# Kernel optimization log

Measured on AMD Instinct MI355X. Metric: run time of the kernel, lower is better.

## Reference

```python
import jax, jax.numpy as jnp
import numpy as np
from jax import lax

B, H, W, C = 16, 56, 56, 256
NH = 8
KD = C // NH  # key/head dim = 32
FF = 1024
EPS = 1e-6
SCALE = KD ** -0.5


def _layernorm(x, g, b):
    m = jnp.mean(x, axis=-1, keepdims=True)
    v = jnp.mean(jnp.square(x - m), axis=-1, keepdims=True)
    return (x - m) * lax.rsqrt(v + EPS) * g + b


def _dwconv(x, w, b):
    # x: (B,H,W,Cd), w: (kh,kw,1,Cd) depthwise (groups = Cd), stride 1, SAME padding
    return lax.conv_general_dilated(
        x, w, window_strides=(1, 1), padding='SAME',
        dimension_numbers=('NHWC', 'HWIO', 'NHWC'),
        feature_group_count=x.shape[-1]) + b


def setup_inputs() -> dict:
    key = jax.random.key(0)
    ks = jax.random.split(key, 20)
    r = lambda i, shape, s=0.02: jax.random.normal(ks[i], shape, jnp.float32) * s
    return {
        'x': jax.random.normal(ks[0], (B, H, W, C), jnp.float32),
        'mask_h': jax.random.normal(ks[1], (NH, H, H), jnp.float32),
        'mask_w': jax.random.normal(ks[2], (NH, W, W), jnp.float32),
        # pos: DWConv2d(C, 3, 1, 1)
        'pos_w': r(3, (3, 3, 1, C)), 'pos_b': jnp.zeros((C,), jnp.float32),
        # retention layer norm
        'ln1_g': jnp.ones((C,), jnp.float32), 'ln1_b': jnp.zeros((C,), jnp.float32),
        # MaSA projections (stored as (in, out) so y = x @ W + b)
        'q_w': r(4, (C, C)), 'q_b': jnp.zeros((C,), jnp.float32),
        'k_w': r(5, (C, C)), 'k_b': jnp.zeros((C,), jnp.float32),
        'v_w': r(6, (C, C)), 'v_b': jnp.zeros((C,), jnp.float32),
        # lepe: DWConv2d(C, 5, 1, 2)
        'lepe_w': r(7, (5, 5, 1, C)), 'lepe_b': jnp.zeros((C,), jnp.float32),
        'out_w': r(8, (C, C)), 'out_b': jnp.zeros((C,), jnp.float32),
        # final layer norm
        'ln2_g': jnp.ones((C,), jnp.float32), 'ln2_b': jnp.zeros((C,), jnp.float32),
        # FFN
        'fc1_w': r(9, (C, FF)), 'fc1_b': jnp.zeros((FF,), jnp.float32),
        'fc2_w': r(10, (FF, C)), 'fc2_b': jnp.zeros((C,), jnp.float32),
    }


def _masa(x, mask_h, mask_w, q_w, q_b, k_w, k_b, v_w, v_b, lepe_w, lepe_b, out_w, out_b):
    b, h, w, _ = x.shape
    q = x @ q_w + q_b
    k = (x @ k_w + k_b) * SCALE
    v = x @ v_w + v_b
    lepe = _dwconv(v, lepe_w, lepe_b)
    qh = q.reshape(b, h, w, NH, KD)
    kh = k.reshape(b, h, w, NH, KD)
    vh = v.reshape(b, h, w, NH, KD)
    # width-axis retention: scores (b, h, NH, w, w), mask_w broadcasts as (NH, w, w)
    attn_w = jax.nn.softmax(jnp.einsum('bhqnd,bhknd->bhnqk', qh, kh) + mask_w, axis=-1)
    vw = jnp.einsum('bhnqk,bhknd->bhnqd', attn_w, vh)  # (b, h, NH, w, KD)
    # height-axis retention: scores (b, w, NH, h, h), mask_h broadcasts as (NH, h, h)
    attn_h = jax.nn.softmax(jnp.einsum('bqwnd,bkwnd->bwnqk', qh, kh) + mask_h, axis=-1)
    out = jnp.einsum('bwnqk,bknwd->bqwnd', attn_h, vw)  # (b, h, w, NH, KD)
    out = out.reshape(b, h, w, NH * KD) + lepe
    return out @ out_w + out_b


def reference(x, mask_h, mask_w, pos_w, pos_b, ln1_g, ln1_b,
              q_w, q_b, k_w, k_b, v_w, v_b, lepe_w, lepe_b, out_w, out_b,
              ln2_g, ln2_b, fc1_w, fc1_b, fc2_w, fc2_b):
    # RetBlock (retention='whole', no layerscale, no dropout / drop_path)
    x = x + _dwconv(x, pos_w, pos_b)
    x = x + _masa(_layernorm(x, ln1_g, ln1_b), mask_h, mask_w,
                  q_w, q_b, k_w, k_b, v_w, v_b, lepe_w, lepe_b, out_w, out_b)
    y = _layernorm(x, ln2_g, ln2_b)
    y = jax.nn.gelu(y @ fc1_w + fc1_b, approximate=False) @ fc2_w + fc2_b
    return x + y
```

## Files before the change

kernel.cpp:

```cpp
#include <hip/hip_runtime.h>
#include <hip/hip_bf16.h>
#include <math.h>
#include <stdint.h>

typedef __bf16 bf16;
typedef __bf16 bf16x8 __attribute__((ext_vector_type(8)));
typedef __bf16 bf16x4 __attribute__((ext_vector_type(4)));
typedef float f32x4 __attribute__((ext_vector_type(4)));

#define AS1 __attribute__((address_space(1)))
#define AS3 __attribute__((address_space(3)))

#define NPIX (16*56*56)
#define CH 256
#define SCALE_K 0.17677669529663687f

__device__ __forceinline__ float gelu_fast(float vv) {
    float t = vv * (-2.30220781f + -0.10294330f * vv * vv);
    float e = __builtin_amdgcn_exp2f(t);
    return vv * __builtin_amdgcn_rcpf(1.0f + e);
}

__global__ __launch_bounds__(256) void prep_kernel(
    const float* __restrict__ q_w, const float* __restrict__ k_w,
    const float* __restrict__ v_w, const float* __restrict__ out_w,
    const float* __restrict__ fc1_w, const float* __restrict__ fc2_w,
    const float* __restrict__ qb, const float* __restrict__ kb,
    const float* __restrict__ vb,
    bf16* __restrict__ wt_qkv, bf16* __restrict__ wt_out,
    bf16* __restrict__ wt_fc1, bf16* __restrict__ wt_fc2,
    float* __restrict__ qkvb)
{
    int idx = blockIdx.x * 256 + threadIdx.x;
    if (idx < 262144) {
        int w = idx >> 16;
        int j = idx & 65535;
        int n = j >> 8, k = j & 255;
        const float* src = (w == 0) ? q_w : (w == 1) ? k_w : (w == 2) ? v_w : out_w;
        float scale = (w == 1) ? SCALE_K : 1.0f;
        bf16* dst = (w < 3) ? (wt_qkv + w * 65536) : wt_out;
        dst[j] = (bf16)(src[k * 256 + n] * scale);
    } else if (idx < 524288) {
        int j = idx - 262144;
        int n = j >> 8, k = j & 255;
        wt_fc1[j] = (bf16)(fc1_w[k * 1024 + n]);
    } else if (idx < 786432) {
        int j = idx - 524288;
        int n = j >> 10, k = j & 1023;
        wt_fc2[j] = (bf16)(fc2_w[k * 256 + n]);
    } else if (idx < 787200) {
        int i = idx - 786432;
        qkvb[i] = (i < 256) ? qb[i] : (i < 512) ? kb[i - 256] * SCALE_K : vb[i - 512];
    }
}

__global__ __launch_bounds__(256) void posconv_ln_kernel(
    const float* __restrict__ x, const float* __restrict__ w,
    const float* __restrict__ bias, const float* __restrict__ g,
    const float* __restrict__ bta, float* __restrict__ x1,
    bf16* __restrict__ tln)
{
    const int wave = threadIdx.x >> 6, lane = threadIdx.x & 63;
    const long pix = (long)blockIdx.x * 4 + wave;
    const int ww = (int)(pix % 56);
    const int hh = (int)((pix / 56) % 56);
    const int b  = (int)(pix / 3136);
    const int c  = lane * 4;
    float4 acc = ((const float4*)(bias + c))[0];
    float4 xin = ((const float4*)(x + pix * 256 + c))[0];
    acc.x += xin.x; acc.y += xin.y; acc.z += xin.z; acc.w += xin.w;
    #pragma unroll
    for (int dh = 0; dh < 3; ++dh) {
        int h2 = hh + dh - 1;
        if (h2 < 0 || h2 >= 56) continue;
        #pragma unroll
        for (int dw = 0; dw < 3; ++dw) {
            int w2 = ww + dw - 1;
            if (w2 < 0 || w2 >= 56) continue;
            float4 xv = ((const float4*)(x + (((long)(b * 56 + h2)) * 56 + w2) * 256 + c))[0];
            float4 wv = ((const float4*)(w + (dh * 3 + dw) * 256 + c))[0];
            acc.x += xv.x * wv.x; acc.y += xv.y * wv.y;
            acc.z += xv.z * wv.z; acc.w += xv.w * wv.w;
        }
    }
    ((float4*)(x1 + pix * 256 + c))[0] = acc;
    float s  = acc.x + acc.y + acc.z + acc.w;
    float q2 = acc.x * acc.x + acc.y * acc.y + acc.z * acc.z + acc.w * acc.w;
    #pragma unroll
    for (int o = 32; o; o >>= 1) {
        s  += __shfl_xor(s,  o, 64);
        q2 += __shfl_xor(q2, o, 64);
    }
    float mean = s * (1.0f / 256.0f);
    float var  = q2 * (1.0f / 256.0f) - mean * mean;
    float rs   = rsqrtf(var + 1e-6f);
    float4 gv = ((const float4*)g)[lane];
    float4 bv = ((const float4*)bta)[lane];
    bf16* o4 = tln + pix * 256 + c;
    o4[0] = (bf16)((acc.x - mean) * rs * gv.x + bv.x);
    o4[1] = (bf16)((acc.y - mean) * rs * gv.y + bv.y);
    o4[2] = (bf16)((acc.z - mean) * rs * gv.z + bv.z);
    o4[3] = (bf16)((acc.w - mean) * rs * gv.w + bv.w);
}

__global__ __launch_bounds__(256) void lepe_kernel(
    const bf16* __restrict__ vpl, const float* __restrict__ w,
    const float* __restrict__ bias, bf16* __restrict__ out)
{
    long idx = (long)blockIdx.x * 256 + threadIdx.x;
    int c8 = (int)(idx & 31);
    long pix = idx >> 5;
    int ww = (int)(pix % 56);
    int hh = (int)((pix / 56) % 56);
    int b  = (int)(pix / 3136);
    int c  = c8 * 8;
    float acc[8];
    #pragma unroll
    for (int j = 0; j < 8; ++j) acc[j] = bias[c + j];
    #pragma unroll
    for (int dh = 0; dh < 5; ++dh) {
        int h2 = hh + dh - 2;
        if (h2 < 0 || h2 >= 56) continue;
        #pragma unroll
        for (int dw = 0; dw < 5; ++dw) {
            int w2 = ww + dw - 2;
            if (w2 < 0 || w2 >= 56) continue;
            bf16x8 vv = *(const bf16x8*)(vpl + (((long)(b * 56 + h2)) * 56 + w2) * 256 + c);
            const float4* wp = (const float4*)(w + (dh * 5 + dw) * 256 + c);
            float4 w0 = wp[0], w1 = wp[1];
            acc[0] += (float)vv[0] * w0.x; acc[1] += (float)vv[1] * w0.y;
            acc[2] += (float)vv[2] * w0.z; acc[3] += (float)vv[3] * w0.w;
            acc[4] += (float)vv[4] * w1.x; acc[5] += (float)vv[5] * w1.y;
            acc[6] += (float)vv[6] * w1.z; acc[7] += (float)vv[7] * w1.w;
        }
    }
    bf16* o = out + pix * 256 + c;
    #pragma unroll
    for (int j = 0; j < 8; ++j) o[j] = (bf16)acc[j];
}

template<bool WIDTH>
__global__ __launch_bounds__(256) void attn_mfma_kernel(
    const bf16* __restrict__ qp, const bf16* __restrict__ kp,
    const bf16* __restrict__ vsrc, const float* __restrict__ mask,
    const bf16* __restrict__ lepe, bf16* __restrict__ outp)
{
    __shared__ bf16 VtAll[4][32][72];
    __shared__ bf16 PlAll[4][16][72];
    const int tid = threadIdx.x;
    const int wave = tid >> 6, lane = tid & 63;
    const int g = lane >> 4, ql = lane & 15;
    const int n  = blockIdx.x / 224;
    const int s  = (blockIdx.x % 224) * 4 + wave;
    const int b  = s / 56, rc = s % 56;
    bf16 (*Vt)[72] = VtAll[wave];
    bf16 (*Pl)[72] = PlAll[wave];
    const long basePix = WIDTH ? ((long)(b * 56 + rc)) * 56 : (long)b * 3136 + rc;
    const long pixStride = WIDTH ? 1 : 56;
    const long stride = pixStride * 256;
    const bf16* qb = qp + basePix * 256 + n * 32;
    const bf16* kb = kp + basePix * 256 + n * 32;
    const bf16* vbp = vsrc + basePix * 256 + n * 32;

    #pragma unroll
    for (int it = 0; it < 2; ++it) {
        int idx = it * 64 + lane;
        if (idx < 112) {
            int pp = idx >> 2, chunk = idx & 3;
            int pos0 = pp * 2;
            bf16x8 v0 = *(const bf16x8*)(vbp + (long)pos0 * stride + chunk * 8);
            bf16x8 v1 = *(const bf16x8*)(vbp + (long)(pos0 + 1) * stride + chunk * 8);
            int colb = pos0 ^ (chunk << 3);
            #pragma unroll
            for (int j = 0; j < 8; ++j) {
                union { bf16 h[2]; unsigned int u; } pk;
                pk.h[0] = v0[j]; pk.h[1] = v1[j];
                *(unsigned int*)&Vt[chunk * 8 + j][colb] = pk.u;
            }
        }
    }
    if (lane < 32) {
        int d = lane;
        int colb = 56 ^ ((d >> 3) << 3);
        *(float4*)&Vt[d][colb] = (float4){0.f, 0.f, 0.f, 0.f};
    }

    bf16x8 qf[4], kf[4];
    #pragma unroll
    for (int t4 = 0; t4 < 4; ++t4) {
        int row = ql + 16 * t4; if (row > 55) row = 55;
        qf[t4] = *(const bf16x8*)(qb + (long)row * stride + 8 * g);
        kf[t4] = *(const bf16x8*)(kb + (long)row * stride + 8 * g);
    }

    f32x4 sA[4][4];
    #pragma unroll
    for (int qt = 0; qt < 4; ++qt)
        #pragma unroll
        for (int kt = 0; kt < 4; ++kt)
            sA[qt][kt] = __builtin_amdgcn_mfma_f32_16x16x32_bf16(
                kf[kt], qf[qt], (f32x4){0.f, 0.f, 0.f, 0.f}, 0, 0, 0);

    const float* mrow = mask + n * 3136;
    #pragma unroll
    for (int qt = 0; qt < 4; ++qt) {
        int qm = ql + 16 * qt; if (qm > 55) qm = 55;
        #pragma unroll
        for (int kt = 0; kt < 4; ++kt) {
            if (kt == 3 && g >= 2) {
                sA[qt][3][0] = -3.0e38f; sA[qt][3][1] = -3.0e38f;
                sA[qt][3][2] = -3.0e38f; sA[qt][3][3] = -3.0e38f;
            } else {
                float4 mv = *(const float4*)(mrow + qm * 56 + kt * 16 + 4 * g);
                sA[qt][kt][0] += mv.x; sA[qt][kt][1] += mv.y;
                sA[qt][kt][2] += mv.z; sA[qt][kt][3] += mv.w;
            }
        }
    }

    #pragma unroll
    for (int qt = 0; qt < 4; ++qt) {
        float m = -3.0e38f;
        #pragma unroll
        for (int kt = 0; kt < 4; ++kt)
            #pragma unroll
            for (int r = 0; r < 4; ++r) m = fmaxf(m, sA[qt][kt][r]);
        m = fmaxf(m, __shfl_xor(m, 16, 64));
        m = fmaxf(m, __shfl_xor(m, 32, 64));
        float p[4][4];
        float sum = 0.f;
        #pragma unroll
        for (int kt = 0; kt < 4; ++kt)
            #pragma unroll
            for (int r = 0; r < 4; ++r) {
                float e = exp2f((sA[qt][kt][r] - m) * 1.4426950408889634f);
                p[kt][r] = e; sum += e;
            }
        sum += __shfl_xor(sum, 16, 64);
        sum += __shfl_xor(sum, 32, 64);
        float rinv = 1.0f / sum;
        #pragma unroll
        for (int kt = 0; kt < 4; ++kt) {
            bf16x4 w;
            #pragma unroll
            for (int r = 0; r < 4; ++r) w[r] = (bf16)(p[kt][r] * rinv);
            *(bf16x4*)&Pl[ql][kt * 16 + 4 * g] = w;
        }
        #pragma unroll
        for (int nt = 0; nt < 2; ++nt) {
            f32x4 o = {0.f, 0.f, 0.f, 0.f};
            #pragma unroll
            for (int ks = 0; ks < 2; ++ks) {
                bf16x8 af = *(const bf16x8*)&Pl[ql][ks * 32 + 8 * g];
                int vrow = ql + 16 * nt;
                int vcol = (ks * 32 + 8 * g) ^ ((vrow >> 3) << 3);
                bf16x8 bv = *(const bf16x8*)&Vt[vrow][vcol];
                o = __builtin_amdgcn_mfma_f32_16x16x32_bf16(af, bv, o, 0, 0, 0);
            }
            if (!(qt == 3 && g >= 2)) {
                #pragma unroll
                for (int r = 0; r < 4; ++r) {
                    int q = 16 * qt + 4 * g + r;
                    long addr = (basePix + (long)q * pixStride) * 256 + n * 32 + nt * 16 + ql;
                    float vv = o[r];
                    if (!WIDTH) vv += (float)lepe[addr];
                    outp[addr] = (bf16)vv;
                }
            }
        }
    }
}

template<bool GELU, bool RESID, bool OUT_BF16, bool QKV3>
__global__ __launch_bounds__(512) void gemm_kernel(
    const bf16* __restrict__ A, const bf16* __restrict__ Wt,
    const float* __restrict__ bias, const float* __restrict__ resid,
    void* __restrict__ Cout, int M, int N, int K)
{
    __shared__ bf16 As[256 * 64];
    __shared__ bf16 Bs[128 * 64];
    const int t = threadIdx.x;
    const int wave = t >> 6, lane = t & 63;
    const int nTilesN = N >> 7;
    const int q8 = gridDim.x >> 3;
    const int o = ((int)blockIdx.x & 7) * q8 + ((int)blockIdx.x >> 3);
    const int tm = o / nTilesN, tn = o % nTilesN;
    const long m0 = (long)tm * 256, n0 = (long)tn * 128;
    const int waveM = (wave >> 1) * 64, waveN = (wave & 1) * 64;
    f32x4 acc[4][4] = {};

    for (int k0 = 0; k0 < K; k0 += 64) {
        #pragma unroll
        for (int i = 0; i < 4; ++i) {
            int c = i * 512 + t;
            int r = c >> 3, cc = (c & 7) * 8;
            const bf16* ga = A + (m0 + r) * (long)K + k0 + cc;
            __builtin_amdgcn_global_load_lds(
                (const AS1 void*)ga, (AS3 void*)(As + c * 8), 16, 0, 0);
        }
        #pragma unroll
        for (int i = 0; i < 2; ++i) {
            int c = i * 512 + t;
            int r = c >> 3, cc = (c & 7) * 8;
            const bf16* gb = Wt + (n0 + r) * (long)K + k0 + cc;
            __builtin_amdgcn_global_load_lds(
                (const AS1 void*)gb, (AS3 void*)(Bs + c * 8), 16, 0, 0);
        }
        __syncthreads();
        #pragma unroll
        for (int kk = 0; kk < 2; ++kk) {
            bf16x8 af[4], bfr[4];
            const int krow = kk * 32 + (lane >> 4) * 8;
            #pragma unroll
            for (int fm = 0; fm < 4; ++fm)
                af[fm] = *(const bf16x8*)&As[(waveM + fm * 16 + (lane & 15)) * 64 + krow];
            #pragma unroll
            for (int fn = 0; fn < 4; ++fn)
                bfr[fn] = *(const bf16x8*)&Bs[(waveN + fn * 16 + (lane & 15)) * 64 + krow];
            #pragma unroll
            for (int fm = 0; fm < 4; ++fm)
                #pragma unroll
                for (int fn = 0; fn < 4; ++fn)
                    acc[fm][fn] = __builtin_amdgcn_mfma_f32_16x16x32_bf16(
                        af[fm], bfr[fn], acc[fm][fn], 0, 0, 0);
        }
        __syncthreads();
    }

    #pragma unroll
    for (int fm = 0; fm < 4; ++fm) {
        #pragma unroll
        for (int r = 0; r < 4; ++r) {
            const long m = m0 + waveM + fm * 16 + (lane >> 4) * 4 + r;
            #pragma unroll
            for (int fn = 0; fn < 4; ++fn) {
                const long n = n0 + waveN + fn * 16 + (lane & 15);
                float vv = acc[fm][fn][r] + bias[n];
                if (GELU)  vv = gelu_fast(vv);
                if (RESID) vv += resid[m * N + n];
                if (QKV3) {
                    long pl = n >> 8;
                    ((bf16*)Cout)[pl * (long)NPIX * 256 + m * 256 + (n & 255)] = (bf16)vv;
                } else if (OUT_BF16) {
                    ((bf16*)Cout)[m * N + n] = (bf16)vv;
                } else {
                    ((float*)Cout)[m * N + n] = vv;
                }
            }
        }
    }
}

__global__ __launch_bounds__(256) void outln_kernel(
    const bf16* __restrict__ A, const bf16* __restrict__ Wt,
    const float* __restrict__ bias, const float* __restrict__ resid,
    const float* __restrict__ g2, const float* __restrict__ b2,
    float* __restrict__ x2out, bf16* __restrict__ uout)
{
    __shared__ bf16 As[64 * 64];
    __shared__ bf16 Bs[256 * 64];
    const int t = threadIdx.x;
    const int wave = t >> 6, lane = t & 63;
    const int g = lane >> 4, ql = lane & 15;
    const int q8 = gridDim.x >> 3;
    const int o = ((int)blockIdx.x & 7) * q8 + ((int)blockIdx.x >> 3);
    const long m0 = (long)o * 64;
    const int waveM = wave * 16;
    f32x4 acc[16] = {};

    for (int k0 = 0; k0 < 256; k0 += 64) {
        #pragma unroll
        for (int i = 0; i < 2; ++i) {
            int c = i * 256 + wave * 64 + lane;
            int r = c >> 3, cc = (c & 7) * 8;
            const bf16* ga = A + (m0 + r) * 256 + k0 + cc;
            __builtin_amdgcn_global_load_lds(
                (const AS1 void*)ga,
                (AS3 void*)(As + (i * 256 + wave * 64) * 8), 16, 0, 0);
        }
        #pragma unroll
        for (int i = 0; i < 8; ++i) {
            int c = i * 256 + wave * 64 + lane;
            int r = c >> 3, cc = (c & 7) * 8;
            const bf16* gb = Wt + r * 256 + k0 + cc;
            __builtin_amdgcn_global_load_lds(
                (const AS1 void*)gb,
                (AS3 void*)(Bs + (i * 256 + wave * 64) * 8), 16, 0, 0);
        }
        __syncthreads();
        #pragma unroll
        for (int kk = 0; kk < 2; ++kk) {
            const int krow = kk * 32 + g * 8;
            bf16x8 af = *(const bf16x8*)&As[(waveM + ql) * 64 + krow];
            #pragma unroll
            for (int fn = 0; fn < 16; ++fn) {
                bf16x8 bv = *(const bf16x8*)&Bs[(fn * 16 + ql) * 64 + krow];
                acc[fn] = __builtin_amdgcn_mfma_f32_16x16x32_bf16(af, bv, acc[fn], 0, 0, 0);
            }
        }
        __syncthreads();
    }

    float rsum[4] = {}, rsq[4] = {};
    #pragma unroll
    for (int fn = 0; fn < 16; ++fn) {
        const int n = fn * 16 + ql;
        const float bn = bias[n];
        #pragma unroll
        for (int r = 0; r < 4; ++r) {
            const long m = m0 + waveM + g * 4 + r;
            float v = acc[fn][r] + bn + resid[m * 256 + n];
            acc[fn][r] = v;
            rsum[r] += v; rsq[r] += v * v;
        }
    }
    #pragma unroll
    for (int r = 0; r < 4; ++r) {
        float s = rsum[r], q = rsq[r];
        #pragma unroll
        for (int off = 8; off; off >>= 1) {
            s += __shfl_xor(s, off, 64);
            q += __shfl_xor(q, off, 64);
        }
        float mean = s * (1.0f / 256.0f);
        float var  = q * (1.0f / 256.0f) - mean * mean;
        rsum[r] = mean;
        rsq[r]  = rsqrtf(var + 1e-6f);
    }
    #pragma unroll
    for (int fn = 0; fn < 16; ++fn) {
        const int n = fn * 16 + ql;
        const float gn = g2[n], bn2 = b2[n];
        #pragma unroll
        for (int r = 0; r < 4; ++r) {
            const long m = m0 + waveM + g * 4 + r;
            float v = acc[fn][r];
            x2out[m * 256 + n] = v;
            uout[m * 256 + n] = (bf16)((v - rsum[r]) * rsq[r] * gn + bn2);
        }
    }
}

extern "C" void kernel_launch(void* const* d_in, const int* in_sizes, int n_in,
                              void* d_out, int out_size, void* d_ws, size_t ws_size,
                              hipStream_t stream)
{
    (void)in_sizes; (void)n_in; (void)out_size; (void)ws_size;
    const float* x      = (const float*)d_in[0];
    const float* mask_h = (const float*)d_in[1];
    const float* mask_w = (const float*)d_in[2];
    const float* pos_w  = (const float*)d_in[3];
    const float* pos_b  = (const float*)d_in[4];
    const float* ln1_g  = (const float*)d_in[5];
    const float* ln1_b  = (const float*)d_in[6];
    const float* q_w    = (const float*)d_in[7];
    const float* q_b    = (const float*)d_in[8];
    const float* k_w    = (const float*)d_in[9];
    const float* k_b    = (const float*)d_in[10];
    const float* v_w    = (const float*)d_in[11];
    const float* v_b    = (const float*)d_in[12];
    const float* lepe_w = (const float*)d_in[13];
    const float* lepe_b = (const float*)d_in[14];
    const float* out_w  = (const float*)d_in[15];
    const float* out_b  = (const float*)d_in[16];
    const float* ln2_g  = (const float*)d_in[17];
    const float* ln2_b  = (const float*)d_in[18];
    const float* fc1_w  = (const float*)d_in[19];
    const float* fc1_b  = (const float*)d_in[20];
    const float* fc2_w  = (const float*)d_in[21];
    const float* fc2_b  = (const float*)d_in[22];

    char* ws = (char*)d_ws;
    size_t off = 0;
    auto alloc = [&](size_t bytes) -> void* {
        void* p = ws + off;
        off += (bytes + 255) & ~(size_t)255;
        return p;
    };
    const int M = NPIX;
    float* x1     = (float*)alloc((size_t)M * 256 * 4);
    bf16*  tln    = (bf16*) alloc((size_t)M * 256 * 2);
    bf16*  qkv3   = (bf16*) alloc((size_t)M * 768 * 2);
    bf16*  lepeb  = (bf16*) alloc((size_t)M * 256 * 2);
    bf16*  vwb    = (bf16*) alloc((size_t)M * 256 * 2);
    bf16*  obuf   = (bf16*) alloc((size_t)M * 256 * 2);
    bf16*  wt_qkv = (bf16*) alloc((size_t)768 * 256 * 2);
    bf16*  wt_out = (bf16*) alloc((size_t)256 * 256 * 2);
    bf16*  wt_fc1 = (bf16*) alloc((size_t)1024 * 256 * 2);
    bf16*  wt_fc2 = (bf16*) alloc((size_t)256 * 1024 * 2);
    float* qkvb   = (float*)alloc(768 * 4);
    bf16*  qpl    = qkv3;
    bf16*  kpl    = qkv3 + (size_t)M * 256;
    bf16*  vpl    = qkv3 + (size_t)M * 512;
    bf16*  h1     = tln;
    float* outf   = (float*)d_out;

    prep_kernel<<<3075, 256, 0, stream>>>(
        q_w, k_w, v_w, out_w, fc1_w, fc2_w, q_b, k_b, v_b,
        wt_qkv, wt_out, wt_fc1, wt_fc2, qkvb);

    posconv_ln_kernel<<<12544, 256, 0, stream>>>(x, pos_w, pos_b, ln1_g, ln1_b, x1, tln);
    gemm_kernel<false, false, true, true><<<196 * 6, 512, 0, stream>>>(
        tln, wt_qkv, qkvb, nullptr, qkv3, M, 768, 256);
    lepe_kernel<<<6272, 256, 0, stream>>>(vpl, lepe_w, lepe_b, lepeb);
    attn_mfma_kernel<true><<<1792, 256, 0, stream>>>(qpl, kpl, vpl, mask_w, nullptr, vwb);
    attn_mfma_kernel<false><<<1792, 256, 0, stream>>>(qpl, kpl, vwb, mask_h, lepeb, obuf);
    outln_kernel<<<784, 256, 0, stream>>>(
        obuf, wt_out, out_b, x1, ln2_g, ln2_b, outf, lepeb);
    gemm_kernel<true, false, true, false><<<196 * 8, 512, 0, stream>>>(
        lepeb, wt_fc1, fc1_b, nullptr, h1, M, 1024, 256);
    gemm_kernel<false, true, false, false><<<196 * 2, 512, 0, stream>>>(
        h1, wt_fc2, fc2_b, outf, outf, M, 256, 1024);
}
```

Before: 403.8 us.

## Merge weight prep into posconv kernel, add MFMA priority hints, enlarge outln tile

Folds the weight-transpose prep work into the position-conv/LayerNorm kernel as extra blocks, removing one launch. Wraps the attention MFMA sequences in s_setprio raises so those waves are favoured during matrix phases. Doubles the out-projection+LayerNorm kernel to 128 rows per block with 512 threads, so each block loads the 256x256 weight tile once for twice as many rows, at the cost of larger LDS use per block.

```diff
diff --git a/kernel.cpp b/kernel.cpp
--- a/kernel.cpp
+++ b/kernel.cpp
@@ -21,7 +21,11 @@
     return vv * __builtin_amdgcn_rcpf(1.0f + e);
 }
 
-__global__ __launch_bounds__(256) void prep_kernel(
+__global__ __launch_bounds__(256) void pre_kernel(
+    const float* __restrict__ x, const float* __restrict__ pos_w,
+    const float* __restrict__ pos_b, const float* __restrict__ ln1_g,
+    const float* __restrict__ ln1_b, float* __restrict__ x1,
+    bf16* __restrict__ tln,
     const float* __restrict__ q_w, const float* __restrict__ k_w,
     const float* __restrict__ v_w, const float* __restrict__ out_w,
     const float* __restrict__ fc1_w, const float* __restrict__ fc2_w,
@@ -31,42 +35,37 @@
     bf16* __restrict__ wt_fc1, bf16* __restrict__ wt_fc2,
     float* __restrict__ qkvb)
 {
-    int idx = blockIdx.x * 256 + threadIdx.x;
-    if (idx < 262144) {
-        int w = idx >> 16;
-        int j = idx & 65535;
-        int n = j >> 8, k = j & 255;
-        const float* src = (w == 0) ? q_w : (w == 1) ? k_w : (w == 2) ? v_w : out_w;
-        float scale = (w == 1) ? SCALE_K : 1.0f;
-        bf16* dst = (w < 3) ? (wt_qkv + w * 65536) : wt_out;
-        dst[j] = (bf16)(src[k * 256 + n] * scale);
-    } else if (idx < 524288) {
-        int j = idx - 262144;
-        int n = j >> 8, k = j & 255;
-        wt_fc1[j] = (bf16)(fc1_w[k * 1024 + n]);
-    } else if (idx < 786432) {
-        int j = idx - 524288;
-        int n = j >> 10, k = j & 1023;
-        wt_fc2[j] = (bf16)(fc2_w[k * 256 + n]);
-    } else if (idx < 787200) {
-        int i = idx - 786432;
-        qkvb[i] = (i < 256) ? qb[i] : (i < 512) ? kb[i - 256] * SCALE_K : vb[i - 512];
-    }
-}
-
-__global__ __launch_bounds__(256) void posconv_ln_kernel(
-    const float* __restrict__ x, const float* __restrict__ w,
-    const float* __restrict__ bias, const float* __restrict__ g,
-    const float* __restrict__ bta, float* __restrict__ x1,
-    bf16* __restrict__ tln)
-{
+    if (blockIdx.x >= 12544) {
+        int idx = (blockIdx.x - 12544) * 256 + threadIdx.x;
+        if (idx < 262144) {
+            int w = idx >> 16;
+            int j = idx & 65535;
+            int n = j >> 8, k = j & 255;
+            const float* src = (w == 0) ? q_w : (w == 1) ? k_w : (w == 2) ? v_w : out_w;
+            float scale = (w == 1) ? SCALE_K : 1.0f;
+            bf16* dst = (w < 3) ? (wt_qkv + w * 65536) : wt_out;
+            dst[j] = (bf16)(src[k * 256 + n] * scale);
+        } else if (idx < 524288) {
+            int j = idx - 262144;
+            int n = j >> 8, k = j & 255;
+            wt_fc1[j] = (bf16)(fc1_w[k * 1024 + n]);
+        } else if (idx < 786432) {
+            int j = idx - 524288;
+            int n = j >> 10, k = j & 1023;
+            wt_fc2[j] = (bf16)(fc2_w[k * 256 + n]);
+        } else if (idx < 787200) {
+            int i = idx - 786432;
+            qkvb[i] = (i < 256) ? qb[i] : (i < 512) ? kb[i - 256] * SCALE_K : vb[i - 512];
+        }
+        return;
+    }
     const int wave = threadIdx.x >> 6, lane = threadIdx.x & 63;
     const long pix = (long)blockIdx.x * 4 + wave;
     const int ww = (int)(pix % 56);
     const int hh = (int)((pix / 56) % 56);
     const int b  = (int)(pix / 3136);
     const int c  = lane * 4;
-    float4 acc = ((const float4*)(bias + c))[0];
+    float4 acc = ((const float4*)(pos_b + c))[0];
     float4 xin = ((const float4*)(x + pix * 256 + c))[0];
     acc.x += xin.x; acc.y += xin.y; acc.z += xin.z; acc.w += xin.w;
     #pragma unroll
@@ -78,7 +77,7 @@
             int w2 = ww + dw - 1;
             if (w2 < 0 || w2 >= 56) continue;
             float4 xv = ((const float4*)(x + (((long)(b * 56 + h2)) * 56 + w2) * 256 + c))[0];
-            float4 wv = ((const float4*)(w + (dh * 3 + dw) * 256 + c))[0];
+            float4 wv = ((const float4*)(pos_w + (dh * 3 + dw) * 256 + c))[0];
             acc.x += xv.x * wv.x; acc.y += xv.y * wv.y;
             acc.z += xv.z * wv.z; acc.w += xv.w * wv.w;
         }
@@ -94,8 +93,8 @@
     float mean = s * (1.0f / 256.0f);
     float var  = q2 * (1.0f / 256.0f) - mean * mean;
     float rs   = rsqrtf(var + 1e-6f);
-    float4 gv = ((const float4*)g)[lane];
-    float4 bv = ((const float4*)bta)[lane];
+    float4 gv = ((const float4*)ln1_g)[lane];
+    float4 bv = ((const float4*)ln1_b)[lane];
     bf16* o4 = tln + pix * 256 + c;
     o4[0] = (bf16)((acc.x - mean) * rs * gv.x + bv.x);
     o4[1] = (bf16)((acc.y - mean) * rs * gv.y + bv.y);
@@ -194,12 +193,14 @@
     }
 
     f32x4 sA[4][4];
+    __builtin_amdgcn_s_setprio(1);
     #pragma unroll
     for (int qt = 0; qt < 4; ++qt)
         #pragma unroll
         for (int kt = 0; kt < 4; ++kt)
             sA[qt][kt] = __builtin_amdgcn_mfma_f32_16x16x32_bf16(
                 kf[kt], qf[qt], (f32x4){0.f, 0.f, 0.f, 0.f}, 0, 0, 0);
+    __builtin_amdgcn_s_setprio(0);
 
     const float* mrow = mask + n * 3136;
     #pragma unroll
@@ -249,6 +250,7 @@
         #pragma unroll
         for (int nt = 0; nt < 2; ++nt) {
             f32x4 o = {0.f, 0.f, 0.f, 0.f};
+            __builtin_amdgcn_s_setprio(1);
             #pragma unroll
             for (int ks = 0; ks < 2; ++ks) {
                 bf16x8 af = *(const bf16x8*)&Pl[ql][ks * 32 + 8 * g];
@@ -257,6 +259,7 @@
                 bf16x8 bv = *(const bf16x8*)&Vt[vrow][vcol];
                 o = __builtin_amdgcn_mfma_f32_16x16x32_bf16(af, bv, o, 0, 0, 0);
             }
+            __builtin_amdgcn_s_setprio(0);
             if (!(qt == 3 && g >= 2)) {
                 #pragma unroll
                 for (int r = 0; r < 4; ++r) {
@@ -351,41 +354,39 @@
     }
 }
 
-__global__ __launch_bounds__(256) void outln_kernel(
+__global__ __launch_bounds__(512) void outln_kernel(
     const bf16* __restrict__ A, const bf16* __restrict__ Wt,
     const float* __restrict__ bias, const float* __restrict__ resid,
     const float* __restrict__ g2, const float* __restrict__ b2,
     float* __restrict__ x2out, bf16* __restrict__ uout)
 {
-    __shared__ bf16 As[64 * 64];
+    __shared__ bf16 As[128 * 64];
     __shared__ bf16 Bs[256 * 64];
     const int t = threadIdx.x;
     const int wave = t >> 6, lane = t & 63;
     const int g = lane >> 4, ql = lane & 15;
     const int q8 = gridDim.x >> 3;
     const int o = ((int)blockIdx.x & 7) * q8 + ((int)blockIdx.x >> 3);
-    const long m0 = (long)o * 64;
+    const long m0 = (long)o * 128;
     const int waveM = wave * 16;
     f32x4 acc[16] = {};
 
     for (int k0 = 0; k0 < 256; k0 += 64) {
         #pragma unroll
         for (int i = 0; i < 2; ++i) {
-            int c = i * 256 + wave * 64 + lane;
+            int c = i * 512 + t;
             int r = c >> 3, cc = (c & 7) * 8;
             const bf16* ga = A + (m0 + r) * 256 + k0 + cc;
             __builtin_amdgcn_global_load_lds(
-                (const AS1 void*)ga,
-                (AS3 void*)(As + (i * 256 + wave * 64) * 8), 16, 0, 0);
-        }
-        #pragma unroll
-        for (int i = 0; i < 8; ++i) {
-            int c = i * 256 + wave * 64 + lane;
+                (const AS1 void*)ga, (AS3 void*)(As + c * 8), 16, 0, 0);
+        }
+        #pragma unroll
+        for (int i = 0; i < 4; ++i) {
+            int c = i * 512 + t;
             int r = c >> 3, cc = (c & 7) * 8;
             const bf16* gb = Wt + r * 256 + k0 + cc;
             __builtin_amdgcn_global_load_lds(
-                (const AS1 void*)gb,
-                (AS3 void*)(Bs + (i * 256 + wave * 64) * 8), 16, 0, 0);
+                (const AS1 void*)gb, (AS3 void*)(Bs + c * 8), 16, 0, 0);
         }
         __syncthreads();
         #pragma unroll
@@ -495,17 +496,17 @@
     bf16*  h1     = tln;
     float* outf   = (float*)d_out;
 
-    prep_kernel<<<3075, 256, 0, stream>>>(
+    pre_kernel<<<12544 + 3075, 256, 0, stream>>>(
+        x, pos_w, pos_b, ln1_g, ln1_b, x1, tln,
         q_w, k_w, v_w, out_w, fc1_w, fc2_w, q_b, k_b, v_b,
         wt_qkv, wt_out, wt_fc1, wt_fc2, qkvb);
 
-    posconv_ln_kernel<<<12544, 256, 0, stream>>>(x, pos_w, pos_b, ln1_g, ln1_b, x1, tln);
     gemm_kernel<false, false, true, true><<<196 * 6, 512, 0, stream>>>(
         tln, wt_qkv, qkvb, nullptr, qkv3, M, 768, 256);
     lepe_kernel<<<6272, 256, 0, stream>>>(vpl, lepe_w, lepe_b, lepeb);
     attn_mfma_kernel<true><<<1792, 256, 0, stream>>>(qpl, kpl, vpl, mask_w, nullptr, vwb);
     attn_mfma_kernel<false><<<1792, 256, 0, stream>>>(qpl, kpl, vwb, mask_h, lepeb, obuf);
-    outln_kernel<<<784, 256, 0, stream>>>(
+    outln_kernel<<<392, 512, 0, stream>>>(
         obuf, wt_out, out_b, x1, ln2_g, ln2_b, outf, lepeb);
     gemm_kernel<true, false, true, false><<<196 * 8, 512, 0, stream>>>(
         lepeb, wt_fc1, fc1_b, nullptr, h1, M, 1024, 256);
```

Result: no change. 400.8 us (-0.8%).
